# Kernel tuning notes

Hardware: AMD Instinct MI355X
Metric: run time of the kernel (lower is better)

## Reference

```python
import jax, jax.numpy as jnp
import numpy as np

N_HOST, N_FLOW, E = 20000, 200000, 600000
D_IN, D_H, D_OUT = 64, 128, 32
NEG_SLOPE = 0.01  # F.leaky_relu default


def setup_inputs() -> dict:
    key = jax.random.key(0)
    ks = jax.random.split(key, 20)

    def w(k, shape):
        # kaiming-uniform-ish init scale (matches Linear fan-in scaling)
        lim = 1.0 / np.sqrt(shape[0])
        return jax.random.uniform(k, shape, jnp.float32, -lim, lim)

    return {
        "x_host": jax.random.normal(ks[0], (N_HOST, D_IN), jnp.float32),
        "x_flow": jax.random.normal(ks[1], (N_FLOW, D_IN), jnp.float32),
        "src_hf": jax.random.randint(ks[2], (E,), 0, N_HOST, dtype=jnp.int32),
        "dst_hf": jax.random.randint(ks[3], (E,), 0, N_FLOW, dtype=jnp.int32),
        "src_fh": jax.random.randint(ks[4], (E,), 0, N_FLOW, dtype=jnp.int32),
        "dst_fh": jax.random.randint(ks[5], (E,), 0, N_HOST, dtype=jnp.int32),
        "W0_hf_l": w(ks[6], (D_IN, D_H)), "W0_hf_r": w(ks[7], (D_IN, D_H)),
        "b0_hf": jnp.zeros((D_H,), jnp.float32),
        "W0_fh_l": w(ks[8], (D_IN, D_H)), "W0_fh_r": w(ks[9], (D_IN, D_H)),
        "b0_fh": jnp.zeros((D_H,), jnp.float32),
        "W1_hf_l": w(ks[10], (D_H, D_H)), "W1_hf_r": w(ks[11], (D_H, D_H)),
        "b1_hf": jnp.zeros((D_H,), jnp.float32),
        "W1_fh_l": w(ks[12], (D_H, D_H)), "W1_fh_r": w(ks[13], (D_H, D_H)),
        "b1_fh": jnp.zeros((D_H,), jnp.float32),
        "W_out": w(ks[14], (D_H, D_OUT)),
        "b_out": jnp.zeros((D_OUT,), jnp.float32),
    }


def _seg_mean(x, src, dst, n_dst):
    """Mean-aggregate src-node features over edges into n_dst segments."""
    s = jax.ops.segment_sum(x[src], dst, num_segments=n_dst)      # [n_dst, d]
    cnt = jax.ops.segment_sum(jnp.ones(src.shape, x.dtype), dst, num_segments=n_dst)
    return s / jnp.clip(cnt, 1.0)[:, None]


def _sage(x_src, x_dst, src, dst, Wl, Wr, b, n_dst):
    # SAGEConv: lin_l(mean_agg) + bias + lin_r(x_dst)
    agg = _seg_mean(x_src, src, dst, n_dst)
    return agg @ Wl + b + x_dst @ Wr


def reference(x_host, x_flow, src_hf, dst_hf, src_fh, dst_fh,
              W0_hf_l, W0_hf_r, b0_hf, W0_fh_l, W0_fh_r, b0_fh,
              W1_hf_l, W1_hf_r, b1_hf, W1_fh_l, W1_fh_r, b1_fh,
              W_out, b_out):
    lrelu = lambda v: jnp.where(v > 0, v, NEG_SLOPE * v)

    # layer 0
    h_flow = lrelu(_sage(x_host, x_flow, src_hf, dst_hf, W0_hf_l, W0_hf_r, b0_hf, N_FLOW))
    h_host = lrelu(_sage(x_flow, x_host, src_fh, dst_fh, W0_fh_l, W0_fh_r, b0_fh, N_HOST))

    # layer 1
    g_flow = lrelu(_sage(h_host, h_flow, src_hf, dst_hf, W1_hf_l, W1_hf_r, b1_hf, N_FLOW))
    g_host = lrelu(_sage(h_flow, h_host, src_fh, dst_fh, W1_fh_l, W1_fh_r, b1_fh, N_HOST))
    del g_host  # computed (matches module) but only 'flow' feeds the head

    return g_flow @ W_out + b_out  # [N_FLOW, D_OUT]
```

## Files before the change

### kernel.cpp

```cpp
#include <hip/hip_runtime.h>


#define N_HOST 20000
#define N_FLOW 200000
#define NEDGE  600000
#define D_IN   64
#define D_H    128
#define D_OUT  32
#define NSEG   (N_FLOW + N_HOST)
#define NBKT_F 196
#define NBKT_H 79
#define NBKT   (NBKT_F + NBKT_H)
#define NEB    586

typedef unsigned short u16;
typedef unsigned int   u32;
typedef short bf16x8 __attribute__((ext_vector_type(8)));
typedef float f32x4  __attribute__((ext_vector_type(4)));
typedef float fx2    __attribute__((ext_vector_type(2)));

__device__ __forceinline__ float bfh(u16 h) { return __uint_as_float(((u32)h) << 16); }
__device__ __forceinline__ u16 fbh(float f) {
    u32 u = __float_as_uint(f);
    return (u16)((u + 0x7fffu + ((u >> 16) & 1u)) >> 16);
}
__device__ __forceinline__ u32 packbf(float x, float y) {
    return (u32)fbh(x) | ((u32)fbh(y) << 16);
}
__device__ __forceinline__ void accp(fx2* a, uint4 u) {
    fx2 p;
    p.x = __uint_as_float(u.x << 16); p.y = __uint_as_float(u.x & 0xffff0000u); a[0] += p;
    p.x = __uint_as_float(u.y << 16); p.y = __uint_as_float(u.y & 0xffff0000u); a[1] += p;
    p.x = __uint_as_float(u.z << 16); p.y = __uint_as_float(u.z & 0xffff0000u); a[2] += p;
    p.x = __uint_as_float(u.w << 16); p.y = __uint_as_float(u.w & 0xffff0000u); a[3] += p;
}
__device__ __forceinline__ uint4 packp(const fx2* a, float inv) {
    uint4 o;
    o.x = packbf(a[0].x * inv, a[0].y * inv);
    o.y = packbf(a[1].x * inv, a[1].y * inv);
    o.z = packbf(a[2].x * inv, a[2].y * inv);
    o.w = packbf(a[3].x * inv, a[3].y * inv);
    return o;
}

__global__ void k_pre(const float* __restrict__ W0_hf_l, const float* __restrict__ W0_hf_r,
                      const float* __restrict__ W0_fh_l, const float* __restrict__ W0_fh_r,
                      const float* __restrict__ W1_l, const float* __restrict__ W1_r,
                      const float* __restrict__ Wout,
                      u16* __restrict__ WT0_hf, u16* __restrict__ WT0_fh,
                      u16* __restrict__ WT1_l, u16* __restrict__ WT1_r,
                      u16* __restrict__ WTo,
                      const float* __restrict__ xf, const float* __restrict__ xh,
                      u16* __restrict__ xfb, u16* __restrict__ xhb,
                      const int* __restrict__ dst_hf, const int* __restrict__ dst_fh,
                      int* __restrict__ bcnt) {
    int b = blockIdx.x, t = threadIdx.x;
    if (b < 34) {
        u16 tmp[8];
        if (b < 32) {
            int e = (b & 7) * 2048 + t * 8;
            int n = e >> 7, k0 = e & 127;
            if (b < 8) {
#pragma unroll
                for (int j = 0; j < 8; j++) {
                    int k = k0 + j;
                    tmp[j] = fbh(k < 64 ? W0_hf_l[k * D_H + n] : W0_hf_r[(k - 64) * D_H + n]);
                }
                *(uint4*)(WT0_hf + n * 128 + k0) = *(uint4*)tmp;
            } else if (b < 16) {
#pragma unroll
                for (int j = 0; j < 8; j++) {
                    int k = k0 + j;
                    tmp[j] = fbh(k < 64 ? W0_fh_l[k * D_H + n] : W0_fh_r[(k - 64) * D_H + n]);
                }
                *(uint4*)(WT0_fh + n * 128 + k0) = *(uint4*)tmp;
            } else if (b < 24) {
#pragma unroll
                for (int j = 0; j < 8; j++) tmp[j] = fbh(W1_l[(k0 + j) * D_H + n]);
                *(uint4*)(WT1_l + n * 128 + k0) = *(uint4*)tmp;
            } else {
#pragma unroll
                for (int j = 0; j < 8; j++) tmp[j] = fbh(W1_r[(k0 + j) * D_H + n]);
                *(uint4*)(WT1_r + n * 128 + k0) = *(uint4*)tmp;
            }
        } else {
            int e = (b - 32) * 2048 + t * 8;
            int n = e >> 7, k0 = e & 127;
#pragma unroll
            for (int j = 0; j < 8; j++) tmp[j] = fbh(Wout[(k0 + j) * D_OUT + n]);
            *(uint4*)(WTo + n * 128 + k0) = *(uint4*)tmp;
        }
    } else if (b < 34 + 6875) {
        int q = (b - 34) * 256 + t;
        const int TF = (N_FLOW * D_IN) / 8;
        const int TT = TF + (N_HOST * D_IN) / 8;
        if (q >= TT) return;
        const float* src; u16* dst; int base;
        if (q < TF) { src = xf; dst = xfb; base = q * 8; }
        else        { src = xh; dst = xhb; base = (q - TF) * 8; }
        float4 f0 = *(const float4*)(src + base);
        float4 f1 = *(const float4*)(src + base + 4);
        uint4 o;
        o.x = packbf(f0.x, f0.y); o.y = packbf(f0.z, f0.w);
        o.z = packbf(f1.x, f1.y); o.w = packbf(f1.z, f1.w);
        *(uint4*)(dst + base) = o;
    } else {
        __shared__ int h[NBKT];
        for (int j = t; j < NBKT; j += 256) h[j] = 0;
        __syncthreads();
        int base = (b - 34 - 6875) * 2048;
#pragma unroll
        for (int i = 0; i < 8; i++) {
            int e = base + t + i * 256;
            if (e < 2 * NEDGE) {
                int bkt = (e < NEDGE) ? (dst_hf[e] >> 10)
                                      : (NBKT_F + (dst_fh[e - NEDGE] >> 8));
                atomicAdd(&h[bkt], 1);
            }
        }
        __syncthreads();
        for (int j = t; j < NBKT; j += 256)
            if (h[j]) atomicAdd(&bcnt[j], h[j]);
    }
}

__global__ void kb2(const int* __restrict__ src_hf, const int* __restrict__ dst_hf,
                    const int* __restrict__ src_fh, const int* __restrict__ dst_fh,
                    const int* __restrict__ bcnt, int* __restrict__ bcur,
                    int2* __restrict__ binE) {
    __shared__ int sp[512];
    __shared__ int lh[NBKT];
    __shared__ int lb[NBKT];
    int t = threadIdx.x;
    int o1 = (t < NBKT) ? bcnt[t] : 0;
    int o2 = (t + 256 < NBKT) ? bcnt[t + 256] : 0;
    sp[t] = o1; sp[t + 256] = o2;
    for (int j = t; j < NBKT; j += 256) lh[j] = 0;
    __syncthreads();
    for (int d = 1; d < 512; d <<= 1) {
        int a0 = (t >= d) ? sp[t - d] : 0;
        int a1 = sp[t + 256 - d];
        __syncthreads();
        sp[t] += a0; sp[t + 256] += a1;
        __syncthreads();
    }
    sp[t] -= o1; sp[t + 256] -= o2;
    __syncthreads();
    int base = blockIdx.x * 2048;
    int mybkt[8], myrank[8], mysrc[8], mydst[8];
#pragma unroll
    for (int i = 0; i < 8; i++) {
        int e = base + t + i * 256;
        mybkt[i] = -1;
        if (e < 2 * NEDGE) {
            int s, d;
            if (e < NEDGE) { s = src_hf[e]; d = dst_hf[e]; }
            else           { s = src_fh[e - NEDGE]; d = dst_fh[e - NEDGE] + N_FLOW; }
            int bkt = (d < N_FLOW) ? (d >> 10) : (NBKT_F + ((d - N_FLOW) >> 8));
            mybkt[i] = bkt; mysrc[i] = s; mydst[i] = d;
            myrank[i] = atomicAdd(&lh[bkt], 1);
        }
    }
    __syncthreads();
    for (int j = t; j < NBKT; j += 256)
        lb[j] = lh[j] ? atomicAdd(&bcur[j], lh[j]) : 0;
    __syncthreads();
#pragma unroll
    for (int i = 0; i < 8; i++) {
        if (mybkt[i] >= 0) {
            int pos = sp[mybkt[i]] + lb[mybkt[i]] + myrank[i];
            binE[pos] = make_int2(mysrc[i], mydst[i]);
        }
    }
}

__global__ __launch_bounds__(256) void kb3(const int2* __restrict__ binE,
                                           const int* __restrict__ bcnt,
                                           int* __restrict__ off, int* __restrict__ csr) {
    __shared__ int sp[512];
    __shared__ int deg[1024];
    __shared__ int ts[256];
    int b = blockIdx.x, t = threadIdx.x;
    sp[t] = (t < NBKT) ? bcnt[t] : 0;
    sp[t + 256] = (t + 256 < NBKT) ? bcnt[t + 256] : 0;
    __syncthreads();
    for (int d = 1; d < 512; d <<= 1) {
        int a0 = (t >= d) ? sp[t - d] : 0;
        int a1 = sp[t + 256 - d];
        __syncthreads();
        sp[t] += a0; sp[t + 256] += a1;
        __syncthreads();
    }
    int e0 = (b == 0) ? 0 : sp[b - 1];
    int e1 = sp[b];
    int nbase, ncnt;
    if (b < NBKT_F) { nbase = b << 10; ncnt = min(1024, N_FLOW - nbase); }
    else { nbase = N_FLOW + ((b - NBKT_F) << 8); ncnt = min(256, NSEG - nbase); }
    for (int i = t; i < 1024; i += 256) deg[i] = 0;
    __syncthreads();
    for (int e = e0 + t; e < e1; e += 256) {
        int2 p = binE[e];
        atomicAdd(&deg[p.y - nbase], 1);
    }
    __syncthreads();
    int loc[4]; int s = 0;
#pragma unroll
    for (int j = 0; j < 4; j++) { loc[j] = s; s += deg[t * 4 + j]; }
    ts[t] = s;
    __syncthreads();
    for (int d = 1; d < 256; d <<= 1) {
        int x = (t >= d) ? ts[t - d] : 0;
        __syncthreads();
        ts[t] += x;
        __syncthreads();
    }
    int base2 = e0 + ts[t] - s;
    int dsave[4];
#pragma unroll
    for (int j = 0; j < 4; j++) dsave[j] = deg[t * 4 + j];
    __syncthreads();
#pragma unroll
    for (int j = 0; j < 4; j++) {
        int idx = t * 4 + j;
        int st = base2 + loc[j];
        deg[idx] = st;
        if (idx < ncnt) off[nbase + idx] = st + dsave[j];
    }
    __syncthreads();
    for (int e = e0 + t; e < e1; e += 256) {
        int2 p = binE[e];
        int r = atomicAdd(&deg[p.y - nbase], 1);
        csr[r] = p.x;
    }
}

__global__ __launch_bounds__(512, 4) void k_host(
    const u16* __restrict__ xfb, const u16* __restrict__ xhb,
    const int* __restrict__ off, const int* __restrict__ csr,
    const u16* __restrict__ WT0, const float* __restrict__ b0,
    const u16* __restrict__ WT1l, u16* __restrict__ hT) {
    __shared__ __align__(16) u16 sA[32 * 136];
    __shared__ __align__(16) float sP[256 * 8];
    __shared__ int sOff[40];
    __shared__ int sCsr[2048];
    const int t = threadIdx.x;
    const int m0 = blockIdx.x * 32;
    if (t < 33) sOff[t] = off[N_FLOW + m0 - 1 + t];
    if (t < 256) {
        int r = t >> 3, c = t & 7;
        uint4 v = *(const uint4*)(xhb + (m0 + r) * 64 + c * 8);
        *(uint4*)(&sA[r * 136 + 64 + c * 8]) = v;
    }
    __syncthreads();
    int st0 = sOff[0];
    int win = sOff[32] - st0;
    bool fit = (win <= 2048);
    if (fit) for (int e = t; e < win; e += 512) sCsr[e] = csr[st0 + e];
    __syncthreads();
    const int r = t >> 4, s8 = (t >> 3) & 1, c = t & 7;
    const int st = sOff[r], en = sOff[r + 1];
    fx2 a[4] = {};
    for (int e = st + s8; e < en; e += 16) {
        int n[8];
#pragma unroll
        for (int j = 0; j < 8; j++) {
            int ee = e + 2 * j;
            n[j] = (ee < en) ? (fit ? sCsr[ee - st0] : csr[ee]) : -1;
        }
        uint4 u[8];
#pragma unroll
        for (int j = 0; j < 8; j++)
            u[j] = (n[j] >= 0) ? *(const uint4*)(xfb + n[j] * 64 + c * 8)
                               : make_uint4(0u, 0u, 0u, 0u);
#pragma unroll
        for (int j = 0; j < 8; j++) accp(a, u[j]);
    }
    if (s8) {
        float4* p = (float4*)(&sP[(r * 8 + c) * 8]);
        p[0] = make_float4(a[0].x, a[0].y, a[1].x, a[1].y);
        p[1] = make_float4(a[2].x, a[2].y, a[3].x, a[3].y);
    }
    __syncthreads();
    if (!s8) {
        const float4* p = (const float4*)(&sP[(r * 8 + c) * 8]);
        float4 v0 = p[0], v1 = p[1];
        a[0].x += v0.x; a[0].y += v0.y; a[1].x += v0.z; a[1].y += v0.w;
        a[2].x += v1.x; a[2].y += v1.y; a[3].x += v1.z; a[3].y += v1.w;
        float inv = (en > st) ? 1.f / (float)(en - st) : 0.f;
        *(uint4*)(&sA[r * 136 + c * 8]) = packp(a, inv);
    }
    __syncthreads();
    const int w = t >> 6, wr = w >> 2, wc = w & 3;
    const int ln = t & 63, l15 = ln & 15, quad = ln >> 4;
    const u16* pA = sA + (wr * 16 + l15) * 136 + quad * 8;
    const u16* pB0 = WT0 + wc * 4096 + l15 * 128 + quad * 8;
    f32x4 acc[2];
    acc[0] = (f32x4){0.f, 0.f, 0.f, 0.f};
    acc[1] = (f32x4){0.f, 0.f, 0.f, 0.f};
#pragma unroll
    for (int s = 0; s < 4; s++) {
        bf16x8 av = *(const bf16x8*)(pA + s * 32);
#pragma unroll
        for (int tt = 0; tt < 2; tt++) {
            bf16x8 b = *(const bf16x8*)(pB0 + tt * 2048 + s * 32);
            acc[tt] = __builtin_amdgcn_mfma_f32_16x16x32_bf16(av, b, acc[tt], 0, 0, 0);
        }
    }
    __syncthreads();
#pragma unroll
    for (int tt = 0; tt < 2; tt++) {
        int col = wc * 32 + tt * 16 + l15;
        float bv = b0[col];
#pragma unroll
        for (int i = 0; i < 4; i++) {
            int rl = wr * 16 + quad * 4 + i;
            float v = acc[tt][i] + bv;
            v = v > 0.f ? v : 0.01f * v;
            sA[rl * 136 + col] = fbh(v);
        }
    }
    __syncthreads();
    const u16* pB1 = WT1l + wc * 4096 + l15 * 128 + quad * 8;
    f32x4 accB[2];
    accB[0] = (f32x4){0.f, 0.f, 0.f, 0.f};
    accB[1] = (f32x4){0.f, 0.f, 0.f, 0.f};
#pragma unroll
    for (int s = 0; s < 4; s++) {
        bf16x8 av = *(const bf16x8*)(pA + s * 32);
#pragma unroll
        for (int tt = 0; tt < 2; tt++) {
            bf16x8 b = *(const bf16x8*)(pB1 + tt * 2048 + s * 32);
            accB[tt] = __builtin_amdgcn_mfma_f32_16x16x32_bf16(av, b, accB[tt], 0, 0, 0);
        }
    }
#pragma unroll
    for (int tt = 0; tt < 2; tt++) {
        int col = wc * 32 + tt * 16 + l15;
#pragma unroll
        for (int i = 0; i < 4; i++) {
            int row = m0 + wr * 16 + quad * 4 + i;
            hT[row * D_H + col] = fbh(accB[tt][i]);
        }
    }
}

__global__ __launch_bounds__(512, 6) void k_mega(
    const u16* __restrict__ xfb, const u16* __restrict__ xhb,
    const int* __restrict__ off, const int* __restrict__ csr,
    const u16* __restrict__ hT,
    const u16* __restrict__ WT0, const float* __restrict__ b0,
    const u16* __restrict__ WT1r, const float* __restrict__ b1,
    const u16* __restrict__ WTo, const float* __restrict__ bout,
    float* __restrict__ OUT) {
    __shared__ __align__(16) u16 sA[64 * 136];
    __shared__ __align__(16) u16 sAg[64 * 136];
    __shared__ int sOff[72];
    __shared__ int sCsr[1024];
    const int t = threadIdx.x;
    const int m0 = blockIdx.x * 64;
    if (t < 65) {
        int idx = m0 - 1 + t;
        sOff[t] = (idx < 0) ? 0 : off[idx];
    }
    {
        int r = t >> 3, c = t & 7;
        uint4 v = *(const uint4*)(xfb + (m0 + r) * 64 + c * 8);
        *(uint4*)(&sA[r * 136 + 64 + c * 8]) = v;
    }
    __syncthreads();
    int st0 = sOff[0];
    int win = sOff[64] - st0;
    bool fit = (win <= 1024);
    if (fit) for (int e = t; e < win; e += 512) sCsr[e] = csr[st0 + e];
    __syncthreads();
    {
        const int r = t >> 3, c = t & 7;
        const int st = sOff[r], en = sOff[r + 1];
        fx2 a0[4] = {}, a1[4] = {}, a2[4] = {};
        for (int e = st; e < en; e += 4) {
            int n[4];
#pragma unroll
            for (int j = 0; j < 4; j++)
                n[j] = (e + j < en) ? (fit ? sCsr[e + j - st0] : csr[e + j]) : -1;
            uint4 ux[4], ua[4], ub[4];
#pragma unroll
            for (int j = 0; j < 4; j++) {
                if (n[j] >= 0) {
                    const u16* px = xhb + n[j] * 64 + c * 8;
                    const u16* ph = hT + n[j] * 128 + c * 16;
                    ux[j] = *(const uint4*)px;
                    ua[j] = *(const uint4*)ph;
                    ub[j] = *(const uint4*)(ph + 8);
                } else {
                    ux[j] = make_uint4(0u, 0u, 0u, 0u);
                    ua[j] = make_uint4(0u, 0u, 0u, 0u);
                    ub[j] = make_uint4(0u, 0u, 0u, 0u);
                }
            }
#pragma unroll
            for (int j = 0; j < 4; j++) {
                accp(a0, ux[j]); accp(a1, ua[j]); accp(a2, ub[j]);
            }
        }
        float inv = (en > st) ? 1.f / (float)(en - st) : 0.f;
        *(uint4*)(&sA[r * 136 + c * 8]) = packp(a0, inv);
        *(uint4*)(&sAg[r * 136 + c * 16]) = packp(a1, inv);
        *(uint4*)(&sAg[r * 136 + c * 16 + 8]) = packp(a2, inv);
    }
    __syncthreads();
    const int w = t >> 6, wr = w >> 1, wc = w & 1;
    const int ln = t & 63, l15 = ln & 15, quad = ln >> 4;
    const u16* pA = sA + (wr * 16 + l15) * 136 + quad * 8;
    const u16* pB0 = WT0 + wc * 8192 + l15 * 128 + quad * 8;
    f32x4 acc[4];
#pragma unroll
    for (int tt = 0; tt < 4; tt++) acc[tt] = (f32x4){0.f, 0.f, 0.f, 0.f};
#pragma unroll
    for (int s = 0; s < 4; s++) {
        bf16x8 av = *(const bf16x8*)(pA + s * 32);
#pragma unroll
        for (int tt = 0; tt < 4; tt++) {
            bf16x8 b = *(const bf16x8*)(pB0 + tt * 2048 + s * 32);
            acc[tt] = __builtin_amdgcn_mfma_f32_16x16x32_bf16(av, b, acc[tt], 0, 0, 0);
        }
    }
    __syncthreads();
#pragma unroll
    for (int tt = 0; tt < 4; tt++) {
        int col = wc * 64 + tt * 16 + l15;
        float bv = b0[col];
#pragma unroll
        for (int i = 0; i < 4; i++) {
            int rl = wr * 16 + quad * 4 + i;
            float v = acc[tt][i] + bv;
            v = v > 0.f ? v : 0.01f * v;
            sA[rl * 136 + col] = fbh(v);
        }
    }
    __syncthreads();
    const u16* pB1 = WT1r + wc * 8192 + l15 * 128 + quad * 8;
    f32x4 accB[4];
#pragma unroll
    for (int tt = 0; tt < 4; tt++) accB[tt] = (f32x4){0.f, 0.f, 0.f, 0.f};
#pragma unroll
    for (int s = 0; s < 4; s++) {
        bf16x8 av = *(const bf16x8*)(pA + s * 32);
#pragma unroll
        for (int tt = 0; tt < 4; tt++) {
            bf16x8 b = *(const bf16x8*)(pB1 + tt * 2048 + s * 32);
            accB[tt] = __builtin_amdgcn_mfma_f32_16x16x32_bf16(av, b, accB[tt], 0, 0, 0);
        }
    }
#pragma unroll
    for (int tt = 0; tt < 4; tt++) {
        int col = wc * 64 + tt * 16 + l15;
        float bv = b1[col];
#pragma unroll
        for (int i = 0; i < 4; i++) {
            int rl = wr * 16 + quad * 4 + i;
            float v = accB[tt][i] + bfh(sAg[rl * 136 + col]) + bv;
            v = v > 0.f ? v : 0.01f * v;
            sAg[rl * 136 + col] = fbh(v);
        }
    }
    __syncthreads();
    const u16* pG = sAg + (wr * 16 + l15) * 136 + quad * 8;
    const u16* pBo = WTo + wc * 2048 + l15 * 128 + quad * 8;
    f32x4 acc2 = (f32x4){0.f, 0.f, 0.f, 0.f};
#pragma unroll
    for (int s = 0; s < 4; s++) {
        bf16x8 g = *(const bf16x8*)(pG + s * 32);
        bf16x8 b = *(const bf16x8*)(pBo + s * 32);
        acc2 = __builtin_amdgcn_mfma_f32_16x16x32_bf16(g, b, acc2, 0, 0, 0);
    }
    {
        int col = wc * 16 + l15;
        float bv = bout[col];
#pragma unroll
        for (int i = 0; i < 4; i++) {
            int row = m0 + wr * 16 + quad * 4 + i;
            OUT[row * D_OUT + col] = acc2[i] + bv;
        }
    }
}

extern "C" void kernel_launch(void* const* d_in, const int* in_sizes, int n_in,
                              void* d_out, int out_size, void* d_ws, size_t ws_size,
                              hipStream_t stream) {
    const float* x_host  = (const float*)d_in[0];
    const float* x_flow  = (const float*)d_in[1];
    const int* src_hf  = (const int*)d_in[2];
    const int* dst_hf  = (const int*)d_in[3];
    const int* src_fh  = (const int*)d_in[4];
    const int* dst_fh  = (const int*)d_in[5];
    const float* W0_hf_l = (const float*)d_in[6];
    const float* W0_hf_r = (const float*)d_in[7];
    const float* b0_hf   = (const float*)d_in[8];
    const float* W0_fh_l = (const float*)d_in[9];
    const float* W0_fh_r = (const float*)d_in[10];
    const float* b0_fh   = (const float*)d_in[11];
    const float* W1_hf_l = (const float*)d_in[12];
    const float* W1_hf_r = (const float*)d_in[13];
    const float* b1_hf   = (const float*)d_in[14];
    const float* W_out   = (const float*)d_in[18];
    const float* b_out   = (const float*)d_in[19];
    float* out = (float*)d_out;

    char* ws = (char*)d_ws;
    int*  off    = (int*)(ws + 0);
    int*  csr    = (int*)(ws + 880000);
    u16*  hT     = (u16*)(ws + 5680000);
    u16*  xfb    = (u16*)(ws + 10800000);
    u16*  xhb    = (u16*)(ws + 36400000);
    int2* binE   = (int2*)(ws + 38960000);
    int*  bcnt   = (int*)(ws + 48560000);
    int*  bcur   = (int*)(ws + 48561280);
    u16*  WT0_hf = (u16*)(ws + 48562560);
    u16*  WT0_fh = (u16*)(ws + 48595328);
    u16*  WT1_l  = (u16*)(ws + 48628096);
    u16*  WT1_r  = (u16*)(ws + 48660864);
    u16*  WTo    = (u16*)(ws + 48693632);

    hipMemsetAsync(bcnt, 0, 2560, stream);
    k_pre<<<34 + 6875 + NEB, 256, 0, stream>>>(
        W0_hf_l, W0_hf_r, W0_fh_l, W0_fh_r, W1_hf_l, W1_hf_r, W_out,
        WT0_hf, WT0_fh, WT1_l, WT1_r, WTo,
        x_flow, x_host, xfb, xhb, dst_hf, dst_fh, bcnt);
    kb2<<<NEB, 256, 0, stream>>>(src_hf, dst_hf, src_fh, dst_fh, bcnt, bcur, binE);
    kb3<<<NBKT, 256, 0, stream>>>(binE, bcnt, off, csr);
    k_host<<<625, 512, 0, stream>>>(xfb, xhb, off, csr, WT0_fh, b0_fh, WT1_l, hT);
    k_mega<<<3125, 512, 0, stream>>>(xfb, xhb, off, csr, hT, WT0_hf, b0_hf,
                                     WT1_r, b1_hf, WTo, b_out, out);
}
```

Measured before the change: 374.4 us.

## Replace bucketed CSR build with per-node degree count, scan and atomic scatter

The CSR construction changes from a two-level bucket sort (bucket histogram, bucket binning into int2 pairs, then a per-bucket local sort) to a direct per-node global atomic degree count, a two-kernel prefix scan and a scatter that fills the CSR with global atomics. This drops the intermediate binE buffer and one full pass over the edges. In exchange it relies on heavy global atomics and a larger memset, and the neighbour order within a node becomes nondeterministic. The k_mega gather is also split into separate per-feature mean loops using a templated helper with fewer live accumulators, and its launch bound is raised from 6 to 8 waves for occupancy.

Result: slower. 432.7 us (+15.6%).

```diff
diff --git a/kernel.cpp b/kernel.cpp
--- a/kernel.cpp
+++ b/kernel.cpp
@@ -8,10 +8,8 @@
 #define D_H    128
 #define D_OUT  32
 #define NSEG   (N_FLOW + N_HOST)
-#define NBKT_F 196
-#define NBKT_H 79
-#define NBKT   (NBKT_F + NBKT_H)
 #define NEB    586
+#define NB_SCAN 108
 
 typedef unsigned short u16;
 typedef unsigned int   u32;
@@ -26,6 +24,16 @@
 }
 __device__ __forceinline__ u32 packbf(float x, float y) {
     return (u32)fbh(x) | ((u32)fbh(y) << 16);
+}
+__device__ __forceinline__ void acc8(float* a, uint4 u) {
+    a[0] += __uint_as_float(u.x << 16);
+    a[1] += __uint_as_float(u.x & 0xffff0000u);
+    a[2] += __uint_as_float(u.y << 16);
+    a[3] += __uint_as_float(u.y & 0xffff0000u);
+    a[4] += __uint_as_float(u.z << 16);
+    a[5] += __uint_as_float(u.z & 0xffff0000u);
+    a[6] += __uint_as_float(u.w << 16);
+    a[7] += __uint_as_float(u.w & 0xffff0000u);
 }
 __device__ __forceinline__ void accp(fx2* a, uint4 u) {
     fx2 p;
@@ -40,6 +48,34 @@
     o.y = packbf(a[1].x * inv, a[1].y * inv);
     o.z = packbf(a[2].x * inv, a[2].y * inv);
     o.w = packbf(a[3].x * inv, a[3].y * inv);
+    return o;
+}
+
+template <int U>
+__device__ __forceinline__ uint4 gmean(const u16* __restrict__ pool, int rs, int coff,
+                                       const int* __restrict__ gcsr,
+                                       const int* __restrict__ lcsr, int st0, bool fit,
+                                       int st, int en) {
+    float a[8] = {0.f, 0.f, 0.f, 0.f, 0.f, 0.f, 0.f, 0.f};
+    for (int e = st; e < en; e += U) {
+        int n[U];
+#pragma unroll
+        for (int j = 0; j < U; j++)
+            n[j] = (e + j < en) ? (fit ? lcsr[e + j - st0] : gcsr[e + j]) : -1;
+        uint4 u[U];
+#pragma unroll
+        for (int j = 0; j < U; j++)
+            u[j] = (n[j] >= 0) ? *(const uint4*)(pool + n[j] * rs + coff)
+                               : make_uint4(0u, 0u, 0u, 0u);
+#pragma unroll
+        for (int j = 0; j < U; j++) acc8(a, u[j]);
+    }
+    float inv = (en > st) ? 1.f / (float)(en - st) : 0.f;
+    uint4 o;
+    o.x = packbf(a[0] * inv, a[1] * inv);
+    o.y = packbf(a[2] * inv, a[3] * inv);
+    o.z = packbf(a[4] * inv, a[5] * inv);
+    o.w = packbf(a[6] * inv, a[7] * inv);
     return o;
 }
 
@@ -53,7 +89,7 @@
                       const float* __restrict__ xf, const float* __restrict__ xh,
                       u16* __restrict__ xfb, u16* __restrict__ xhb,
                       const int* __restrict__ dst_hf, const int* __restrict__ dst_fh,
-                      int* __restrict__ bcnt) {
+                      int* __restrict__ deg) {
     int b = blockIdx.x, t = threadIdx.x;
     if (b < 34) {
         u16 tmp[8];
@@ -105,133 +141,107 @@
         o.z = packbf(f1.x, f1.y); o.w = packbf(f1.z, f1.w);
         *(uint4*)(dst + base) = o;
     } else {
-        __shared__ int h[NBKT];
-        for (int j = t; j < NBKT; j += 256) h[j] = 0;
-        __syncthreads();
         int base = (b - 34 - 6875) * 2048;
 #pragma unroll
         for (int i = 0; i < 8; i++) {
             int e = base + t + i * 256;
             if (e < 2 * NEDGE) {
-                int bkt = (e < NEDGE) ? (dst_hf[e] >> 10)
-                                      : (NBKT_F + (dst_fh[e - NEDGE] >> 8));
-                atomicAdd(&h[bkt], 1);
+                int node = (e < NEDGE) ? dst_hf[e] : (N_FLOW + dst_fh[e - NEDGE]);
+                atomicAdd(&deg[node], 1);
             }
         }
+    }
+}
+
+__global__ __launch_bounds__(512) void k_scan1(const int* __restrict__ deg,
+                                               int* __restrict__ off,
+                                               int* __restrict__ bsum) {
+    __shared__ int ts[512];
+    int b = blockIdx.x, t = threadIdx.x;
+    int base = b * 2048 + t * 4;
+    int4 d = make_int4(0, 0, 0, 0);
+    if (base + 3 < NSEG) d = *(const int4*)(deg + base);
+    else if (base < NSEG) {
+        d.x = deg[base];
+        if (base + 1 < NSEG) d.y = deg[base + 1];
+        if (base + 2 < NSEG) d.z = deg[base + 2];
+    }
+    int l1 = d.x + d.y, l2 = l1 + d.z, l3 = l2 + d.w;
+    ts[t] = l3;
+    __syncthreads();
+    for (int s = 1; s < 512; s <<= 1) {
+        int v = (t >= s) ? ts[t - s] : 0;
         __syncthreads();
-        for (int j = t; j < NBKT; j += 256)
-            if (h[j]) atomicAdd(&bcnt[j], h[j]);
-    }
-}
-
-__global__ void kb2(const int* __restrict__ src_hf, const int* __restrict__ dst_hf,
-                    const int* __restrict__ src_fh, const int* __restrict__ dst_fh,
-                    const int* __restrict__ bcnt, int* __restrict__ bcur,
-                    int2* __restrict__ binE) {
-    __shared__ int sp[512];
-    __shared__ int lh[NBKT];
-    __shared__ int lb[NBKT];
-    int t = threadIdx.x;
-    int o1 = (t < NBKT) ? bcnt[t] : 0;
-    int o2 = (t + 256 < NBKT) ? bcnt[t + 256] : 0;
-    sp[t] = o1; sp[t + 256] = o2;
-    for (int j = t; j < NBKT; j += 256) lh[j] = 0;
-    __syncthreads();
-    for (int d = 1; d < 512; d <<= 1) {
-        int a0 = (t >= d) ? sp[t - d] : 0;
-        int a1 = sp[t + 256 - d];
+        ts[t] += v;
         __syncthreads();
-        sp[t] += a0; sp[t + 256] += a1;
+    }
+    int add = ts[t] - l3;
+    if (base + 3 < NSEG) {
+        *(int4*)(off + base) = make_int4(add + d.x, add + l1, add + l2, add + l3);
+    } else if (base < NSEG) {
+        off[base] = add + d.x;
+        if (base + 1 < NSEG) off[base + 1] = add + l1;
+        if (base + 2 < NSEG) off[base + 2] = add + l2;
+    }
+    if (t == 511) bsum[b] = ts[511];
+}
+
+__global__ __launch_bounds__(512) void k_scan2(const int* __restrict__ deg,
+                                               int* __restrict__ off,
+                                               const int* __restrict__ bsum,
+                                               int* __restrict__ cur) {
+    __shared__ int red[512];
+    int b = blockIdx.x, t = threadIdx.x;
+    red[t] = (t < b) ? bsum[t] : 0;
+    __syncthreads();
+    for (int s = 256; s > 0; s >>= 1) {
+        if (t < s) red[t] += red[t + s];
         __syncthreads();
     }
-    sp[t] -= o1; sp[t + 256] -= o2;
-    __syncthreads();
-    int base = blockIdx.x * 2048;
-    int mybkt[8], myrank[8], mysrc[8], mydst[8];
-#pragma unroll
-    for (int i = 0; i < 8; i++) {
-        int e = base + t + i * 256;
-        mybkt[i] = -1;
-        if (e < 2 * NEDGE) {
-            int s, d;
-            if (e < NEDGE) { s = src_hf[e]; d = dst_hf[e]; }
-            else           { s = src_fh[e - NEDGE]; d = dst_fh[e - NEDGE] + N_FLOW; }
-            int bkt = (d < N_FLOW) ? (d >> 10) : (NBKT_F + ((d - N_FLOW) >> 8));
-            mybkt[i] = bkt; mysrc[i] = s; mydst[i] = d;
-            myrank[i] = atomicAdd(&lh[bkt], 1);
-        }
-    }
-    __syncthreads();
-    for (int j = t; j < NBKT; j += 256)
-        lb[j] = lh[j] ? atomicAdd(&bcur[j], lh[j]) : 0;
-    __syncthreads();
-#pragma unroll
-    for (int i = 0; i < 8; i++) {
-        if (mybkt[i] >= 0) {
-            int pos = sp[mybkt[i]] + lb[mybkt[i]] + myrank[i];
-            binE[pos] = make_int2(mysrc[i], mydst[i]);
-        }
-    }
-}
-
-__global__ __launch_bounds__(256) void kb3(const int2* __restrict__ binE,
-                                           const int* __restrict__ bcnt,
-                                           int* __restrict__ off, int* __restrict__ csr) {
-    __shared__ int sp[512];
-    __shared__ int deg[1024];
-    __shared__ int ts[256];
-    int b = blockIdx.x, t = threadIdx.x;
-    sp[t] = (t < NBKT) ? bcnt[t] : 0;
-    sp[t + 256] = (t + 256 < NBKT) ? bcnt[t + 256] : 0;
-    __syncthreads();
-    for (int d = 1; d < 512; d <<= 1) {
-        int a0 = (t >= d) ? sp[t - d] : 0;
-        int a1 = sp[t + 256 - d];
-        __syncthreads();
-        sp[t] += a0; sp[t + 256] += a1;
-        __syncthreads();
-    }
-    int e0 = (b == 0) ? 0 : sp[b - 1];
-    int e1 = sp[b];
-    int nbase, ncnt;
-    if (b < NBKT_F) { nbase = b << 10; ncnt = min(1024, N_FLOW - nbase); }
-    else { nbase = N_FLOW + ((b - NBKT_F) << 8); ncnt = min(256, NSEG - nbase); }
-    for (int i = t; i < 1024; i += 256) deg[i] = 0;
-    __syncthreads();
-    for (int e = e0 + t; e < e1; e += 256) {
-        int2 p = binE[e];
-        atomicAdd(&deg[p.y - nbase], 1);
-    }
-    __syncthreads();
-    int loc[4]; int s = 0;
-#pragma unroll
-    for (int j = 0; j < 4; j++) { loc[j] = s; s += deg[t * 4 + j]; }
-    ts[t] = s;
-    __syncthreads();
-    for (int d = 1; d < 256; d <<= 1) {
-        int x = (t >= d) ? ts[t - d] : 0;
-        __syncthreads();
-        ts[t] += x;
-        __syncthreads();
-    }
-    int base2 = e0 + ts[t] - s;
-    int dsave[4];
-#pragma unroll
-    for (int j = 0; j < 4; j++) dsave[j] = deg[t * 4 + j];
-    __syncthreads();
-#pragma unroll
-    for (int j = 0; j < 4; j++) {
-        int idx = t * 4 + j;
-        int st = base2 + loc[j];
-        deg[idx] = st;
-        if (idx < ncnt) off[nbase + idx] = st + dsave[j];
-    }
-    __syncthreads();
-    for (int e = e0 + t; e < e1; e += 256) {
-        int2 p = binE[e];
-        int r = atomicAdd(&deg[p.y - nbase], 1);
-        csr[r] = p.x;
-    }
+    int add = red[0];
+    int base = b * 2048 + t * 4;
+    if (base >= NSEG) return;
+    if (base + 3 < NSEG) {
+        int4 o = *(const int4*)(off + base);
+        int4 d = *(const int4*)(deg + base);
+        o.x += add; o.y += add; o.z += add; o.w += add;
+        *(int4*)(off + base) = o;
+        *(int4*)(cur + base) = make_int4(o.x - d.x, o.y - d.y, o.z - d.z, o.w - d.w);
+    } else {
+#pragma unroll
+        for (int j = 0; j < 4; j++) {
+            if (base + j < NSEG) {
+                int o = off[base + j] + add;
+                off[base + j] = o;
+                cur[base + j] = o - deg[base + j];
+            }
+        }
+    }
+}
+
+__global__ __launch_bounds__(512) void k_scat(const int* __restrict__ src_hf,
+                                              const int* __restrict__ dst_hf,
+                                              const int* __restrict__ src_fh,
+                                              const int* __restrict__ dst_fh,
+                                              int* __restrict__ cur,
+                                              int* __restrict__ csr) {
+    int e = blockIdx.x * 2048 + threadIdx.x * 4;
+    if (e >= 2 * NEDGE) return;
+    int4 s4, d4; int nb;
+    if (e < NEDGE) {
+        s4 = *(const int4*)(src_hf + e);
+        d4 = *(const int4*)(dst_hf + e);
+        nb = 0;
+    } else {
+        s4 = *(const int4*)(src_fh + e - NEDGE);
+        d4 = *(const int4*)(dst_fh + e - NEDGE);
+        nb = N_FLOW;
+    }
+    int p0 = atomicAdd(&cur[d4.x + nb], 1);
+    int p1 = atomicAdd(&cur[d4.y + nb], 1);
+    int p2 = atomicAdd(&cur[d4.z + nb], 1);
+    int p3 = atomicAdd(&cur[d4.w + nb], 1);
+    csr[p0] = s4.x; csr[p1] = s4.y; csr[p2] = s4.z; csr[p3] = s4.w;
 }
 
 __global__ __launch_bounds__(512, 4) void k_host(
@@ -344,7 +354,7 @@
     }
 }
 
-__global__ __launch_bounds__(512, 6) void k_mega(
+__global__ __launch_bounds__(512, 8) void k_mega(
     const u16* __restrict__ xfb, const u16* __restrict__ xhb,
     const int* __restrict__ off, const int* __restrict__ csr,
     const u16* __restrict__ hT,
@@ -374,38 +384,16 @@
     if (fit) for (int e = t; e < win; e += 512) sCsr[e] = csr[st0 + e];
     __syncthreads();
     {
-        const int r = t >> 3, c = t & 7;
-        const int st = sOff[r], en = sOff[r + 1];
-        fx2 a0[4] = {}, a1[4] = {}, a2[4] = {};
-        for (int e = st; e < en; e += 4) {
-            int n[4];
-#pragma unroll
-            for (int j = 0; j < 4; j++)
-                n[j] = (e + j < en) ? (fit ? sCsr[e + j - st0] : csr[e + j]) : -1;
-            uint4 ux[4], ua[4], ub[4];
-#pragma unroll
-            for (int j = 0; j < 4; j++) {
-                if (n[j] >= 0) {
-                    const u16* px = xhb + n[j] * 64 + c * 8;
-                    const u16* ph = hT + n[j] * 128 + c * 16;
-                    ux[j] = *(const uint4*)px;
-                    ua[j] = *(const uint4*)ph;
-                    ub[j] = *(const uint4*)(ph + 8);
-                } else {
-                    ux[j] = make_uint4(0u, 0u, 0u, 0u);
-                    ua[j] = make_uint4(0u, 0u, 0u, 0u);
-                    ub[j] = make_uint4(0u, 0u, 0u, 0u);
-                }
-            }
-#pragma unroll
-            for (int j = 0; j < 4; j++) {
-                accp(a0, ux[j]); accp(a1, ua[j]); accp(a2, ub[j]);
-            }
-        }
-        float inv = (en > st) ? 1.f / (float)(en - st) : 0.f;
-        *(uint4*)(&sA[r * 136 + c * 8]) = packp(a0, inv);
-        *(uint4*)(&sAg[r * 136 + c * 16]) = packp(a1, inv);
-        *(uint4*)(&sAg[r * 136 + c * 16 + 8]) = packp(a2, inv);
+        int r = t >> 3, c = t & 7;
+        uint4 o = gmean<4>(xhb, 64, c * 8, csr, sCsr, st0, fit, sOff[r], sOff[r + 1]);
+        *(uint4*)(&sA[r * 136 + c * 8]) = o;
+    }
+#pragma unroll
+    for (int i = 0; i < 2; i++) {
+        int q = t + i * 512;
+        int r = q >> 4, c = q & 15;
+        uint4 o = gmean<4>(hT, 128, c * 8, csr, sCsr, st0, fit, sOff[r], sOff[r + 1]);
+        *(uint4*)(&sAg[r * 136 + c * 8]) = o;
     }
     __syncthreads();
     const int w = t >> 6, wr = w >> 1, wc = w & 1;
@@ -512,22 +500,23 @@
     u16*  hT     = (u16*)(ws + 5680000);
     u16*  xfb    = (u16*)(ws + 10800000);
     u16*  xhb    = (u16*)(ws + 36400000);
-    int2* binE   = (int2*)(ws + 38960000);
-    int*  bcnt   = (int*)(ws + 48560000);
-    int*  bcur   = (int*)(ws + 48561280);
+    int*  deg    = (int*)(ws + 38960000);
+    int*  cur    = (int*)(ws + 39840000);
+    int*  bsum   = (int*)(ws + 40720000);
     u16*  WT0_hf = (u16*)(ws + 48562560);
     u16*  WT0_fh = (u16*)(ws + 48595328);
     u16*  WT1_l  = (u16*)(ws + 48628096);
     u16*  WT1_r  = (u16*)(ws + 48660864);
     u16*  WTo    = (u16*)(ws + 48693632);
 
-    hipMemsetAsync(bcnt, 0, 2560, stream);
+    hipMemsetAsync(deg, 0, 880000, stream);
     k_pre<<<34 + 6875 + NEB, 256, 0, stream>>>(
         W0_hf_l, W0_hf_r, W0_fh_l, W0_fh_r, W1_hf_l, W1_hf_r, W_out,
         WT0_hf, WT0_fh, WT1_l, WT1_r, WTo,
-        x_flow, x_host, xfb, xhb, dst_hf, dst_fh, bcnt);
-    kb2<<<NEB, 256, 0, stream>>>(src_hf, dst_hf, src_fh, dst_fh, bcnt, bcur, binE);
-    kb3<<<NBKT, 256, 0, stream>>>(binE, bcnt, off, csr);
+        x_flow, x_host, xfb, xhb, dst_hf, dst_fh, deg);
+    k_scan1<<<NB_SCAN, 512, 0, stream>>>(deg, off, bsum);
+    k_scan2<<<NB_SCAN, 512, 0, stream>>>(deg, off, bsum, cur);
+    k_scat<<<NEB, 512, 0, stream>>>(src_hf, dst_hf, src_fh, dst_fh, cur, csr);
     k_host<<<625, 512, 0, stream>>>(xfb, xhb, off, csr, WT0_fh, b0_fh, WT1_l, hT);
     k_mega<<<3125, 512, 0, stream>>>(xfb, xhb, off, csr, hT, WT0_hf, b0_hf,
                                      WT1_r, b1_hf, WTo, b_out, out);
```
